# Kernel optimization log

Measured on AMD Instinct MI355X. Metric: run time of the kernel, lower is better.

## Reference

```python
import jax, jax.numpy as jnp
import numpy as np

E, R, CIN, COUT = 8, 8, 256, 256
B, H, W = 16, 64, 64
DN = ('NCHW', 'OIHW', 'NCHW')


def setup_inputs() -> dict:
    key = jax.random.key(0)
    k1, k2, k3, k4 = jax.random.split(key, 4)
    x = jax.random.normal(k1, (B, CIN, H, W), jnp.float32)
    probs = jax.nn.softmax(jax.random.normal(k2, (E,), jnp.float32))
    # in conv: rank filters over in_channels, kernel (1,3); out conv: kernel (3,1)
    weight_in = jax.random.normal(k3, (E, R, CIN, 1, 3), jnp.float32) * 0.02
    weight_out = jax.random.normal(k4, (E, COUT, R, 3, 1), jnp.float32) * 0.02
    return {"x": x, "probs": probs, "weight_in": weight_in, "weight_out": weight_out}


def _expert_conv(x, w_in, w_out):
    # in conv: stride (1,1), padding (0,1) -> [B,R,H,W]
    h = jax.lax.conv_general_dilated(x, w_in, window_strides=(1, 1),
                                     padding=[(0, 0), (1, 1)], dimension_numbers=DN)
    # out conv: stride (1,1), padding (1,0) -> [B,COUT,H,W]
    return jax.lax.conv_general_dilated(h, w_out, window_strides=(1, 1),
                                        padding=[(1, 1), (0, 0)], dimension_numbers=DN)


def reference(x, probs, weight_in, weight_out):
    # vmap over experts replaces the Python loop; outs: [E,B,COUT,H,W]
    outs = jax.vmap(lambda wi, wo: _expert_conv(x, wi, wo))(weight_in, weight_out)
    # probability-weighted sum over experts (stack + sum in the original)
    return jnp.einsum('e,ebchw->bchw', probs, outs)
```

## Files before the change

### kernel.cpp

```cpp
#include <hip/hip_runtime.h>
#include <hip/hip_bf16.h>


typedef __bf16 bf16x8 __attribute__((ext_vector_type(8)));
typedef __bf16 bf16x4 __attribute__((ext_vector_type(4)));
typedef float  f32x4  __attribute__((ext_vector_type(4)));
typedef float  f32x4v __attribute__((ext_vector_type(4)));

#define CIN_  256
#define COUT_ 256
#define M1    64
#define K1    768
#define K2    192
#define CS    264
#define HS    200

static __device__ __forceinline__ unsigned short f2bf(float f) {
    union { float f; unsigned u; } v; v.f = f;
    unsigned r = v.u + 0x7FFFu + ((v.u >> 16) & 1u);
    return (unsigned short)(r >> 16);
}

__global__ void prep_weights(const float* __restrict__ probs,
                             const float* __restrict__ w_in,
                             const float* __restrict__ w_out,
                             unsigned short* __restrict__ W1,
                             unsigned short* __restrict__ W2,
                             unsigned short* __restrict__ hT) {
    int idx = blockIdx.x * blockDim.x + threadIdx.x;
    if (idx < M1 * K1) {
        int er = idx / K1, rem = idx % K1;
        int kx = rem / CIN_, c = rem % CIN_;
        int e = er >> 3;
        W1[idx] = f2bf(probs[e] * w_in[(er * CIN_ + c) * 3 + kx]);
    } else if (idx < 2 * M1 * K1) {
        int i2 = idx - M1 * K1;
        int o = i2 / K2, rem = i2 % K2;
        if (rem < K2) {
            int ky = rem / M1, er = rem % M1;
            int e = er >> 3, r = er & 7;
            W2[i2] = f2bf(w_out[((e * COUT_ + o) * 8 + r) * 3 + ky]);
        }
    } else {
        int i3 = idx - 2 * M1 * K1;
        if (i3 < 16384) {
            int b = i3 >> 10, r = i3 & 1023;
            int yp = (r >> 9) * 65;
            int col = (r & 511) * 8;
            bf16x8 z = {};
            *(bf16x8*)(hT + ((b * 66 + yp) * 4096) + col) = z;
        }
    }
}

__global__ __launch_bounds__(256)
void conv_in_kernel(const float* __restrict__ x,
                    const unsigned short* __restrict__ W1,
                    unsigned short* __restrict__ hT) {
    __shared__ unsigned short xs[66 * CS];
    const int bid  = blockIdx.x;
    const int b    = bid >> 6, y = bid & 63;
    const int tid  = threadIdx.x;
    const int lane = tid & 63;
    const int wave = tid >> 6;
    const int g    = lane >> 4;
    const int lr   = lane & 15;

    if (tid < 66) {
        int row = (tid < 33) ? 0 : 65;
        int col = (tid - (tid < 33 ? 0 : 33)) * 8;
        bf16x4 z4 = {};
        *(bf16x4*)&xs[row * CS + col] = z4;
        *(bf16x4*)&xs[row * CS + col + 4] = z4;
    }

    const int cb = tid & 31;
    const int n0 = (tid >> 5) << 3;
    const float* xp = x + (((b * CIN_ + cb * 8) * 64 + y) * 64 + n0);
    f32x4v va[8], vb[8];
    #pragma unroll
    for (int i = 0; i < 8; ++i) {
        va[i] = *(const f32x4v*)(xp + i * 4096);
        vb[i] = *(const f32x4v*)(xp + i * 4096 + 4);
    }
    #pragma unroll
    for (int j = 0; j < 4; ++j) {
        bf16x8 r0, r1;
        #pragma unroll
        for (int i = 0; i < 8; ++i) { r0[i] = (__bf16)va[i][j]; r1[i] = (__bf16)vb[i][j]; }
        *(bf16x8*)&xs[(n0 + j + 1) * CS + cb * 8] = r0;
        *(bf16x8*)&xs[(n0 + j + 5) * CS + cb * 8] = r1;
    }
    __syncthreads();

    f32x4 acc[4];
    #pragma unroll
    for (int i = 0; i < 4; ++i) acc[i] = (f32x4){0.f, 0.f, 0.f, 0.f};

    const unsigned short* w1p = W1 + (wave * 16 + lr) * K1 + g * 8;
    #pragma unroll
    for (int cc = 0; cc < 8; ++cc) {
        #pragma unroll
        for (int kx = 0; kx < 3; ++kx) {
            bf16x8 af = *(const bf16x8*)(w1p + kx * CIN_ + cc * 32);
            #pragma unroll
            for (int nt = 0; nt < 4; ++nt) {
                bf16x8 bf = *(const bf16x8*)&xs[(nt * 16 + lr + kx) * CS + cc * 32 + g * 8];
                acc[nt] = __builtin_amdgcn_mfma_f32_16x16x32_bf16(af, bf, acc[nt], 0, 0, 0);
            }
        }
    }
    unsigned short* hp = hT + ((b * 66 + y + 1) * 64) * 64;
    #pragma unroll
    for (int nt = 0; nt < 4; ++nt) {
        int n = nt * 16 + lr;
        bf16x4 pk;
        #pragma unroll
        for (int r2 = 0; r2 < 4; ++r2) pk[r2] = (__bf16)acc[nt][r2];
        *(bf16x4*)&hp[n * 64 + wave * 16 + g * 4] = pk;
    }
}

__global__ __launch_bounds__(256)
void conv_out_kernel(const unsigned short* __restrict__ hT,
                     const unsigned short* __restrict__ W2,
                     float* __restrict__ out) {
    __shared__ unsigned short hs[64 * HS];
    const int bid  = blockIdx.x;
    const int b    = bid >> 6, y = bid & 63;
    const int tid  = threadIdx.x;
    const int lane = tid & 63;
    const int wave = tid >> 6;
    const int g    = lane >> 4;
    const int lr   = lane & 15;

    if (tid < 192) {
        int ky = tid >> 6, xr = tid & 63;
        const unsigned short* src = hT + (((b * 66) + y + ky) * 64 + xr) * 64;
        unsigned short* dst = &hs[xr * HS + ky * 64];
        #pragma unroll
        for (int j = 0; j < 8; ++j)
            *(bf16x8*)&dst[j * 8] = *(const bf16x8*)&src[j * 8];
    }
    __syncthreads();

    f32x4 acc[4][4];
    #pragma unroll
    for (int ot = 0; ot < 4; ++ot)
        #pragma unroll
        for (int nt = 0; nt < 4; ++nt) acc[ot][nt] = (f32x4){0.f, 0.f, 0.f, 0.f};

    #pragma unroll
    for (int kc = 0; kc < 6; ++kc) {
        bf16x8 bfrag[4];
        #pragma unroll
        for (int nt = 0; nt < 4; ++nt)
            bfrag[nt] = *(const bf16x8*)&hs[(nt * 16 + lr) * HS + kc * 32 + g * 8];
        #pragma unroll
        for (int ot = 0; ot < 4; ++ot) {
            bf16x8 af = *(const bf16x8*)(W2 + ((wave * 4 + ot) * 16 + lr) * K2 +
                                         kc * 32 + g * 8);
            #pragma unroll
            for (int nt = 0; nt < 4; ++nt)
                acc[ot][nt] = __builtin_amdgcn_mfma_f32_16x16x32_bf16(af, bfrag[nt],
                                                                      acc[ot][nt], 0, 0, 0);
        }
    }

    #pragma unroll
    for (int ot = 0; ot < 4; ++ot) {
        #pragma unroll
        for (int r2 = 0; r2 < 4; ++r2) {
            int o = (wave * 4 + ot) * 16 + g * 4 + r2;
            float* orow = out + ((b * COUT_ + o) * 64 + y) * 64;
            #pragma unroll
            for (int nt = 0; nt < 4; ++nt)
                orow[nt * 16 + lr] = acc[ot][nt][r2];
        }
    }
}

extern "C" void kernel_launch(void* const* d_in, const int* in_sizes, int n_in,
                              void* d_out, int out_size, void* d_ws, size_t ws_size,
                              hipStream_t stream) {
    const float* x     = (const float*)d_in[0];
    const float* probs = (const float*)d_in[1];
    const float* w_in  = (const float*)d_in[2];
    const float* w_out = (const float*)d_in[3];
    float* out = (float*)d_out;

    unsigned short* W1 = (unsigned short*)d_ws;
    unsigned short* W2 = W1 + M1 * K1;
    unsigned short* hT = W2 + COUT_ * K2;

    prep_weights<<<(2 * M1 * K1 + 16384 + 255) / 256, 256, 0, stream>>>(
        probs, w_in, w_out, W1, W2, hT);
    conv_in_kernel<<<16 * 64, 256, 0, stream>>>(x, W1, hT);
    conv_out_kernel<<<16 * 64, 256, 0, stream>>>(hT, W2, out);
}
```

Baseline: 57.83 us.

## Coalesce input staging with swizzled LDS stores and spread hT loads across threads

The conv_in staging now reads each channel row with contiguous float4 loads across threads. It transposes into shared memory through single bf16 stores at an XOR-swizzled column, and the MFMA loop reads from the matching swizzled addresses. conv_out spreads the hT-to-LDS copy across all 256 threads instead of 192 threads doing 8 loads each. Both kernels get a launch-bounds occupancy hint of 4. The aim is better global coalescing and fewer LDS bank conflicts, at the cost of many more scalar 16-bit LDS writes and possible register pressure from the hint.

```diff
diff --git a/kernel.cpp b/kernel.cpp
--- a/kernel.cpp
+++ b/kernel.cpp
@@ -5,7 +5,6 @@
 typedef __bf16 bf16x8 __attribute__((ext_vector_type(8)));
 typedef __bf16 bf16x4 __attribute__((ext_vector_type(4)));
 typedef float  f32x4  __attribute__((ext_vector_type(4)));
-typedef float  f32x4v __attribute__((ext_vector_type(4)));
 
 #define CIN_  256
 #define COUT_ 256
@@ -36,11 +35,9 @@
     } else if (idx < 2 * M1 * K1) {
         int i2 = idx - M1 * K1;
         int o = i2 / K2, rem = i2 % K2;
-        if (rem < K2) {
-            int ky = rem / M1, er = rem % M1;
-            int e = er >> 3, r = er & 7;
-            W2[i2] = f2bf(w_out[((e * COUT_ + o) * 8 + r) * 3 + ky]);
-        }
+        int ky = rem / M1, er = rem % M1;
+        int e = er >> 3, r = er & 7;
+        W2[i2] = f2bf(w_out[((e * COUT_ + o) * 8 + r) * 3 + ky]);
     } else {
         int i3 = idx - 2 * M1 * K1;
         if (i3 < 16384) {
@@ -53,7 +50,7 @@
     }
 }
 
-__global__ __launch_bounds__(256)
+__global__ __launch_bounds__(256, 4)
 void conv_in_kernel(const float* __restrict__ x,
                     const unsigned short* __restrict__ W1,
                     unsigned short* __restrict__ hT) {
@@ -74,22 +71,26 @@
         *(bf16x4*)&xs[row * CS + col + 4] = z4;
     }
 
-    const int cb = tid & 31;
-    const int n0 = (tid >> 5) << 3;
-    const float* xp = x + (((b * CIN_ + cb * 8) * 64 + y) * 64 + n0);
-    f32x4v va[8], vb[8];
-    #pragma unroll
-    for (int i = 0; i < 8; ++i) {
-        va[i] = *(const f32x4v*)(xp + i * 4096);
-        vb[i] = *(const f32x4v*)(xp + i * 4096 + 4);
-    }
-    #pragma unroll
-    for (int j = 0; j < 4; ++j) {
-        bf16x8 r0, r1;
-        #pragma unroll
-        for (int i = 0; i < 8; ++i) { r0[i] = (__bf16)va[i][j]; r1[i] = (__bf16)vb[i][j]; }
-        *(bf16x8*)&xs[(n0 + j + 1) * CS + cb * 8] = r0;
-        *(bf16x8*)&xs[(n0 + j + 5) * CS + cb * 8] = r1;
+    const int crow = tid >> 4;
+    const int n4   = (tid & 15) << 2;
+    const int swzt = (tid & 7) << 3;
+    const float* xbase = x + ((b * CIN_ + crow) * 64 + y) * 64 + n4;
+    unsigned short* wr = &xs[(n4 + 1) * CS];
+
+    #pragma unroll
+    for (int r = 0; r < 4; ++r) {
+        float4 ld[4];
+        #pragma unroll
+        for (int q = 0; q < 4; ++q)
+            ld[q] = *(const float4*)(xbase + (r * 4 + q) * 16 * 4096);
+        #pragma unroll
+        for (int q = 0; q < 4; ++q) {
+            int cx = ((r * 4 + q) * 16 + crow) ^ swzt;
+            wr[0 * CS + cx] = f2bf(ld[q].x);
+            wr[1 * CS + cx] = f2bf(ld[q].y);
+            wr[2 * CS + cx] = f2bf(ld[q].z);
+            wr[3 * CS + cx] = f2bf(ld[q].w);
+        }
     }
     __syncthreads();
 
@@ -99,15 +100,31 @@
 
     const unsigned short* w1p = W1 + (wave * 16 + lr) * K1 + g * 8;
     #pragma unroll
-    for (int cc = 0; cc < 8; ++cc) {
-        #pragma unroll
-        for (int kx = 0; kx < 3; ++kx) {
-            bf16x8 af = *(const bf16x8*)(w1p + kx * CIN_ + cc * 32);
-            #pragma unroll
-            for (int nt = 0; nt < 4; ++nt) {
-                bf16x8 bf = *(const bf16x8*)&xs[(nt * 16 + lr + kx) * CS + cc * 32 + g * 8];
-                acc[nt] = __builtin_amdgcn_mfma_f32_16x16x32_bf16(af, bf, acc[nt], 0, 0, 0);
-            }
+    for (int kx = 0; kx < 3; ++kx) {
+        bf16x8 af[8];
+        #pragma unroll
+        for (int cc = 0; cc < 8; ++cc)
+            af[cc] = *(const bf16x8*)(w1p + kx * CIN_ + cc * 32);
+        int ns0 = lr + kx;
+        int sz0 = (((ns0 - 1) >> 2) & 7) << 3;
+        int ns1 = ns0 + 16, sz1 = (((ns1 - 1) >> 2) & 7) << 3;
+        int ns2 = ns0 + 32, sz2 = (((ns2 - 1) >> 2) & 7) << 3;
+        int ns3 = ns0 + 48, sz3 = (((ns3 - 1) >> 2) & 7) << 3;
+        const unsigned short* r0 = &xs[ns0 * CS];
+        const unsigned short* r1 = &xs[ns1 * CS];
+        const unsigned short* r2p = &xs[ns2 * CS];
+        const unsigned short* r3 = &xs[ns3 * CS];
+        #pragma unroll
+        for (int cc = 0; cc < 8; ++cc) {
+            int co = cc * 32 + g * 8;
+            acc[0] = __builtin_amdgcn_mfma_f32_16x16x32_bf16(
+                af[cc], *(const bf16x8*)&r0[co ^ sz0], acc[0], 0, 0, 0);
+            acc[1] = __builtin_amdgcn_mfma_f32_16x16x32_bf16(
+                af[cc], *(const bf16x8*)&r1[co ^ sz1], acc[1], 0, 0, 0);
+            acc[2] = __builtin_amdgcn_mfma_f32_16x16x32_bf16(
+                af[cc], *(const bf16x8*)&r2p[co ^ sz2], acc[2], 0, 0, 0);
+            acc[3] = __builtin_amdgcn_mfma_f32_16x16x32_bf16(
+                af[cc], *(const bf16x8*)&r3[co ^ sz3], acc[3], 0, 0, 0);
         }
     }
     unsigned short* hp = hT + ((b * 66 + y + 1) * 64) * 64;
@@ -121,7 +138,7 @@
     }
 }
 
-__global__ __launch_bounds__(256)
+__global__ __launch_bounds__(256, 4)
 void conv_out_kernel(const unsigned short* __restrict__ hT,
                      const unsigned short* __restrict__ W2,
                      float* __restrict__ out) {
@@ -134,13 +151,14 @@
     const int g    = lane >> 4;
     const int lr   = lane & 15;
 
-    if (tid < 192) {
-        int ky = tid >> 6, xr = tid & 63;
-        const unsigned short* src = hT + (((b * 66) + y + ky) * 64 + xr) * 64;
-        unsigned short* dst = &hs[xr * HS + ky * 64];
-        #pragma unroll
-        for (int j = 0; j < 8; ++j)
-            *(bf16x8*)&dst[j * 8] = *(const bf16x8*)&src[j * 8];
+    const int rrow = tid >> 3;
+    const int u8   = (tid & 7) * 8;
+    #pragma unroll
+    for (int v = 0; v < 6; ++v) {
+        int R  = v * 32 + rrow;
+        int ky = R >> 6, xr = R & 63;
+        const unsigned short* src = hT + (((b * 66) + y + ky) * 64 + xr) * 64 + u8;
+        *(bf16x8*)&hs[xr * HS + ky * 64 + u8] = *(const bf16x8*)src;
     }
     __syncthreads();
 
```

Result: faster. 56.66 us (-2.0%).
